# Kernel optimization log

Measured on AMD Instinct MI355X. Metric: run time of the kernel, lower is better.

## Reference

```python
import jax, jax.numpy as jnp
import numpy as np


def setup_inputs() -> dict:
    key = jax.random.key(0)
    k1, k2, k3, k4 = jax.random.split(key, 4)
    bs, n, f_in, f_out, n_head = 4, 2048, 64, 64, 8
    h = jax.random.normal(k1, (bs, n, f_in), dtype=jnp.float32)
    adj = jnp.ones((bs, n, n), dtype=bool)  # accepted by forward but unused
    # xavier-uniform-like init scales
    w = jax.random.uniform(k2, (n_head, f_in, f_out), dtype=jnp.float32,
                           minval=-1.0, maxval=1.0) * np.sqrt(6.0 / (f_in + f_out))
    a_src = jax.random.uniform(k3, (n_head, f_out, 1), dtype=jnp.float32,
                               minval=-1.0, maxval=1.0) * np.sqrt(6.0 / (f_out + 1))
    a_dst = jax.random.uniform(k4, (n_head, f_out, 1), dtype=jnp.float32,
                               minval=-1.0, maxval=1.0) * np.sqrt(6.0 / (f_out + 1))
    bias_p = jnp.zeros((f_out,), dtype=jnp.float32)
    return {"h": h, "adj": adj, "w": w, "a_src": a_src, "a_dst": a_dst, "bias_p": bias_p}


def reference(h, adj, w, a_src, a_dst, bias_p):
    # h: [b, n, f_in], w: [h, f_in, f_out]
    h_prime = jnp.einsum('bnf,hfo->bhno', h, w)          # [b, h, n, f_out]
    t = jnp.tanh(h_prime)
    attn_src = jnp.einsum('bhno,ho->bhn', t, a_src[..., 0])  # [b, h, n]
    attn_dst = jnp.einsum('bhno,ho->bhn', t, a_dst[..., 0])  # [b, h, n]
    # attn[b,h,i,j] = src[b,h,i] + dst[b,h,j]  (dense; adj unused in original)
    attn = attn_src[..., :, None] + attn_dst[..., None, :]   # [b, h, n, n]
    attn = jnp.where(attn >= 0, attn, 0.2 * attn)            # leaky_relu(0.2)
    attn = jax.nn.softmax(attn, axis=-1)
    # dropout p=0.0 -> identity
    out = jnp.einsum('bhij,bhjo->bhio', attn, h_prime)       # [b, h, n, f_out]
    return out + bias_p
```

## Files before the change

### kernel.cpp

```cpp
#include <hip/hip_runtime.h>
#include <hip/hip_bf16.h>

#define NN 2048
#define FF 64
#define NH 8
#define BDIM 4
#define BH 32

typedef __attribute__((ext_vector_type(8))) short short8;
typedef __attribute__((ext_vector_type(4))) float floatx4;
typedef __attribute__((ext_vector_type(4))) unsigned uint4v;

__device__ __forceinline__ float LDIN(const void* p, size_t i, int b16) {
    return b16 ? __bfloat162float(((const __hip_bfloat16*)p)[i]) : ((const float*)p)[i];
}
__device__ __forceinline__ unsigned packhi(float f0, float f1) {
    return __builtin_amdgcn_perm(__float_as_uint(f1), __float_as_uint(f0), 0x07060302);
}
__device__ __forceinline__ float hitrunc(float x) {
    return __uint_as_float(__float_as_uint(x) & 0xFFFF0000u);
}
__device__ __forceinline__ ushort bf16bits(float v) {
    __hip_bfloat16 b = __float2bfloat16(v);
    return __builtin_bit_cast(ushort, b);
}

__global__ __launch_bounds__(256) void k_proj(
    const void* __restrict__ h, const void* __restrict__ w,
    const void* __restrict__ asrc, const void* __restrict__ adst,
    ushort* __restrict__ hpTt, float* __restrict__ esHa, float* __restrict__ esLa,
    float* __restrict__ edHa, float* __restrict__ edLa, int* __restrict__ flagOut)
{
    const int t  = threadIdx.x;
    const int rt = blockIdx.x & 31;
    const int hd = (blockIdx.x >> 5) & 7;
    const int b  = blockIdx.x >> 8;
    const int bh = b * NH + hd;
    const int r0 = rt * 64;

    __shared__ int sb16;
    __shared__ ushort SH[4 * 64 * 72];
    ushort* bHi = SH;
    ushort* bLo = SH + 64 * 72;
    ushort* aHi = SH + 2 * 64 * 72;
    ushort* aLo = SH + 3 * 64 * 72;

    if (t < 64) {
        unsigned word = ((const unsigned*)h)[t];
        unsigned lowexp = (word >> 7) & 0xFFu;
        bool plaus = (lowexp >= 96u && lowexp <= 159u);
        unsigned long long m = __ballot(plaus);
        if (t == 0) sb16 = (__popcll(m) >= 48) ? 1 : 0;
    }
    __syncthreads();
    const int b16 = sb16;
    if (blockIdx.x == 0 && t == 0) flagOut[0] = b16;

    const int lane = t & 63, wv = t >> 6;
    const int ml = lane & 15, q = lane >> 4;

    if (b16) {
        const ushort* wp = (const ushort*)w + (size_t)hd * FF * FF;
        const int n = t & 63, kq4 = (t >> 6) * 4;
#pragma unroll
        for (int g = 0; g < 4; ++g) {
            int kb = g * 16 + kq4;
            ushort v0 = wp[(kb + 0) * FF + n];
            ushort v1 = wp[(kb + 1) * FF + n];
            ushort v2 = wp[(kb + 2) * FF + n];
            ushort v3 = wp[(kb + 3) * FF + n];
            uint2 pk = { (unsigned)v0 | ((unsigned)v1 << 16),
                         (unsigned)v2 | ((unsigned)v3 << 16) };
            *(uint2*)&bHi[n * 72 + kb] = pk;
        }
        const ushort* hsrc = (const ushort*)h + (size_t)(b * NN + r0) * FF;
        for (int g = t; g < 512; g += 256) {
            int row = g >> 3, c8 = (g & 7) * 8;
            uint4v u = *(const uint4v*)(hsrc + row * FF + c8);
            *(uint4v*)&aHi[row * 72 + c8] = u;
        }
    } else {
        const float* wp = (const float*)w + (size_t)hd * FF * FF;
        const int n = t & 63, kq4 = (t >> 6) * 4;
#pragma unroll
        for (int g = 0; g < 4; ++g) {
            int kb = g * 16 + kq4;
            float x0 = wp[(kb + 0) * FF + n];
            float x1 = wp[(kb + 1) * FF + n];
            float x2 = wp[(kb + 2) * FF + n];
            float x3 = wp[(kb + 3) * FF + n];
            uint2 hi2 = { packhi(x0, x1), packhi(x2, x3) };
            uint2 lo2 = { packhi(x0 - hitrunc(x0), x1 - hitrunc(x1)),
                          packhi(x2 - hitrunc(x2), x3 - hitrunc(x3)) };
            *(uint2*)&bHi[n * 72 + kb] = hi2;
            *(uint2*)&bLo[n * 72 + kb] = lo2;
        }
        const float* hsrc = (const float*)h + (size_t)(b * NN + r0) * FF;
        for (int g = t; g < 1024; g += 256) {
            int row = g >> 4, c4 = (g & 15) * 4;
            floatx4 x = *(const floatx4*)(hsrc + row * FF + c4);
            uint2 hi2 = { packhi(x[0], x[1]), packhi(x[2], x[3]) };
            uint2 lo2 = { packhi(x[0] - hitrunc(x[0]), x[1] - hitrunc(x[1])),
                          packhi(x[2] - hitrunc(x[2]), x[3] - hitrunc(x[3])) };
            *(uint2*)&aHi[row * 72 + c4] = hi2;
            *(uint2*)&aLo[row * 72 + c4] = lo2;
        }
    }
    __syncthreads();

    short8 ah[2], al[2];
#pragma unroll
    for (int kc = 0; kc < 2; ++kc) {
        ah[kc] = *(const short8*)&aHi[(wv * 16 + ml) * 72 + kc * 32 + q * 8];
        if (!b16) al[kc] = *(const short8*)&aLo[(wv * 16 + ml) * 72 + kc * 32 + q * 8];
    }
    short8 bhf[4][2], blf[4][2];
#pragma unroll
    for (int nt = 0; nt < 4; ++nt)
#pragma unroll
        for (int kc = 0; kc < 2; ++kc) {
            bhf[nt][kc] = *(const short8*)&bHi[(nt * 16 + ml) * 72 + kc * 32 + q * 8];
            if (!b16) blf[nt][kc] = *(const short8*)&bLo[(nt * 16 + ml) * 72 + kc * 32 + q * 8];
        }

    float aS[4], aD[4];
#pragma unroll
    for (int nt = 0; nt < 4; ++nt) {
        aS[nt] = LDIN(asrc, hd * FF + nt * 16 + ml, b16);
        aD[nt] = LDIN(adst, hd * FF + nt * 16 + ml, b16);
    }

    floatx4 acc[4];
#pragma unroll
    for (int nt = 0; nt < 4; ++nt) {
        floatx4 a = {0.f, 0.f, 0.f, 0.f};
        if (b16) {
#pragma unroll
            for (int kc = 0; kc < 2; ++kc)
                a = __builtin_amdgcn_mfma_f32_16x16x32_bf16(ah[kc], bhf[nt][kc], a, 0, 0, 0);
        } else {
#pragma unroll
            for (int kc = 0; kc < 2; ++kc) {
                a = __builtin_amdgcn_mfma_f32_16x16x32_bf16(ah[kc], bhf[nt][kc], a, 0, 0, 0);
                a = __builtin_amdgcn_mfma_f32_16x16x32_bf16(ah[kc], blf[nt][kc], a, 0, 0, 0);
                a = __builtin_amdgcn_mfma_f32_16x16x32_bf16(al[kc], bhf[nt][kc], a, 0, 0, 0);
            }
        }
        acc[nt] = a;
    }

    __syncthreads();
    ushort* trans = SH;
#pragma unroll
    for (int nt = 0; nt < 4; ++nt) {
        ushort b0 = bf16bits(acc[nt][0]), b1 = bf16bits(acc[nt][1]);
        ushort b2 = bf16bits(acc[nt][2]), b3 = bf16bits(acc[nt][3]);
        uint2 pk = { (unsigned)b0 | ((unsigned)b1 << 16),
                     (unsigned)b2 | ((unsigned)b3 << 16) };
        *(uint2*)&trans[(nt * 16 + ml) * 72 + wv * 16 + q * 4] = pk;
    }

    float ps[4] = {0.f, 0.f, 0.f, 0.f}, pd[4] = {0.f, 0.f, 0.f, 0.f};
#pragma unroll
    for (int nt = 0; nt < 4; ++nt)
#pragma unroll
        for (int reg = 0; reg < 4; ++reg) {
            float tv = tanhf(acc[nt][reg]);
            ps[reg] += tv * aS[nt];
            pd[reg] += tv * aD[nt];
        }
#pragma unroll
    for (int msk = 1; msk < 16; msk <<= 1)
#pragma unroll
        for (int reg = 0; reg < 4; ++reg) {
            ps[reg] += __shfl_xor(ps[reg], msk, 64);
            pd[reg] += __shfl_xor(pd[reg], msk, 64);
        }
    if (ml == 0) {
#pragma unroll
        for (int reg = 0; reg < 4; ++reg) {
            int i = bh * NN + r0 + wv * 16 + q * 4 + reg;
            float sv = ps[reg], dv = pd[reg];
            esHa[i] = __expf(sv);
            esLa[i] = __expf(0.2f * sv);
            edHa[i] = __expf(dv);
            edLa[i] = __expf(0.2f * dv);
        }
    }
    __syncthreads();
    {
        const int o = t >> 2, part = (t & 3) * 16;
        uint4v v0 = *(const uint4v*)&trans[o * 72 + part];
        uint4v v1 = *(const uint4v*)&trans[o * 72 + part + 8];
        ushort* dst = hpTt + (((size_t)bh * 32 + rt) * 64 + o) * 64 + part;
        *(uint4v*)dst = v0;
        *(uint4v*)(dst + 8) = v1;
    }
}

__global__ __launch_bounds__(256) void k_attn(
    const ushort* __restrict__ hpTt,
    const float* __restrict__ esHa, const float* __restrict__ esLa,
    const float* __restrict__ edHa, const float* __restrict__ edLa,
    const void* __restrict__ bias, const int* __restrict__ flag,
    void* __restrict__ out)
{
    const int b16 = flag[0];
    const int t = threadIdx.x;
    const int wv = t >> 6, lane = t & 63;
    const int ml = lane & 15, q = lane >> 4;
    const int bh = blockIdx.x & 31;
    const int ibase = (blockIdx.x >> 5) * 128;
    const int i0 = ibase + wv * 16;

    __shared__ ushort Bc[2][64 * 72];

    const ushort* src = hpTt + (size_t)bh * NN * FF;
    const float* ehp = edHa + bh * NN;
    const float* elp = edLa + bh * NN;

    float es[2], es2[2];
#pragma unroll
    for (int it = 0; it < 2; ++it) {
        es[it]  = esHa[bh * NN + i0 + it * 64 + ml];
        es2[it] = esLa[bh * NN + i0 + it * 64 + ml];
    }

    floatx4 acc[2][4];
#pragma unroll
    for (int it = 0; it < 2; ++it)
#pragma unroll
        for (int nt = 0; nt < 4; ++nt) acc[it][nt] = (floatx4){0.f, 0.f, 0.f, 0.f};
    float den[2] = {0.f, 0.f};

    auto stage = [&](int c, int buf) {
        const ushort* s = src + (size_t)c * 4096 + t * 16;
        uint4v u0 = *(const uint4v*)s;
        uint4v u1 = *(const uint4v*)(s + 8);
        ushort* d = &Bc[buf][(t >> 2) * 72 + (t & 3) * 16];
        *(uint4v*)d = u0;
        *(uint4v*)(d + 8) = u1;
    };

    auto compute = [&](int c, int buf) {
        const int j0 = c * 64;
#pragma unroll
        for (int ks = 0; ks < 2; ++ks) {
            const int col = ks * 32 + q * 8;
            floatx4 eh0 = *(const floatx4*)(ehp + j0 + col);
            floatx4 eh1 = *(const floatx4*)(ehp + j0 + col + 4);
            floatx4 el0 = *(const floatx4*)(elp + j0 + col);
            floatx4 el1 = *(const floatx4*)(elp + j0 + col + 4);
            short8 Bf[4];
#pragma unroll
            for (int nt = 0; nt < 4; ++nt)
                Bf[nt] = *(const short8*)&Bc[buf][(nt * 16 + ml) * 72 + col];
#pragma unroll
            for (int it = 0; it < 2; ++it) {
                float p[8];
#pragma unroll
                for (int j = 0; j < 4; ++j) {
                    p[j]     = fmaxf(es[it] * eh0[j], es2[it] * el0[j]);
                    p[j + 4] = fmaxf(es[it] * eh1[j], es2[it] * el1[j]);
                }
                den[it] += ((p[0] + p[1]) + (p[2] + p[3]))
                         + ((p[4] + p[5]) + (p[6] + p[7]));
                unsigned hw[4], lw[4];
#pragma unroll
                for (int pr = 0; pr < 4; ++pr) {
                    float a0 = p[2 * pr], a1 = p[2 * pr + 1];
                    hw[pr] = packhi(a0, a1);
                    lw[pr] = packhi(a0 - hitrunc(a0), a1 - hitrunc(a1));
                }
                short8 PH = __builtin_bit_cast(short8, (uint4v){hw[0], hw[1], hw[2], hw[3]});
                short8 PL = __builtin_bit_cast(short8, (uint4v){lw[0], lw[1], lw[2], lw[3]});
#pragma unroll
                for (int nt = 0; nt < 4; ++nt) {
                    acc[it][nt] = __builtin_amdgcn_mfma_f32_16x16x32_bf16(PH, Bf[nt], acc[it][nt], 0, 0, 0);
                    acc[it][nt] = __builtin_amdgcn_mfma_f32_16x16x32_bf16(PL, Bf[nt], acc[it][nt], 0, 0, 0);
                }
            }
        }
    };

    stage(0, 0);
    __syncthreads();
    for (int c = 0; c < 32; ++c) {
        const int buf = c & 1;
        if (c < 31) stage(c + 1, buf ^ 1);
        compute(c, buf);
        __syncthreads();
    }

    float biasv[4];
#pragma unroll
    for (int nt = 0; nt < 4; ++nt) biasv[nt] = LDIN(bias, nt * 16 + ml, b16);

#pragma unroll
    for (int it = 0; it < 2; ++it) {
        float d2 = den[it];
        d2 += __shfl_xor(d2, 16, 64);
        d2 += __shfl_xor(d2, 32, 64);
#pragma unroll
        for (int reg = 0; reg < 4; ++reg) {
            float dr = __shfl(d2, q * 4 + reg, 64);
            float inv = 1.0f / dr;
            int i = i0 + it * 64 + q * 4 + reg;
#pragma unroll
            for (int nt = 0; nt < 4; ++nt) {
                float val = acc[it][nt][reg] * inv + biasv[nt];
                size_t oi = ((size_t)bh * NN + i) * FF + nt * 16 + ml;
                if (b16) ((__hip_bfloat16*)out)[oi] = __float2bfloat16(val);
                else     ((float*)out)[oi] = val;
            }
        }
    }
}

extern "C" void kernel_launch(void* const* d_in, const int* in_sizes, int n_in,
                              void* d_out, int out_size, void* d_ws, size_t ws_size,
                              hipStream_t stream) {
    const void* h    = d_in[0];
    const void* w    = d_in[2];
    const void* asrc = d_in[3];
    const void* adst = d_in[4];
    const void* bias = d_in[5];

    float* ws = (float*)d_ws;
    int*    flag = (int*)ws;
    ushort* hpTt = (ushort*)(ws + 16);
    float*  esHa = (float*)(hpTt + (size_t)BH * NN * FF);
    float*  esLa = esHa + BH * NN;
    float*  edHa = esLa + BH * NN;
    float*  edLa = edHa + BH * NN;

    k_proj<<<BDIM * NH * 32, 256, 0, stream>>>(h, w, asrc, adst,
                                               hpTt, esHa, esLa, edHa, edLa, flag);
    k_attn<<<BH * 16, 256, 0, stream>>>(hpTt, esHa, esLa, edHa, edLa,
                                        bias, flag, d_out);
}
```

Measured before the change: 161.5 us.

## Rescale softmax by source factor, drop low-bf16 split, use MFMA for denominator

The attention kernel factors the per-row source exponential out of the softmax, since it cancels in the normalization, leaving one multiply per element against a precomputed exp(-0.8*src) ratio. It drops the hi/lo bf16 split of the probabilities, keeping one MFMA per tile instead of two, and computes the denominator with an extra MFMA against a ones vector. Destination exponentials are staged into shared memory, blocks grow to 512 threads with one row-tile per wave, LDS padding is replaced with an XOR swizzle, and tanh uses an exp/rcp approximation. The changes cut ALU and MFMA work but lower precision of the attention weights to a single bf16 term.

```diff
diff --git a/kernel.cpp b/kernel.cpp
--- a/kernel.cpp
+++ b/kernel.cpp
@@ -24,11 +24,18 @@
     __hip_bfloat16 b = __float2bfloat16(v);
     return __builtin_bit_cast(ushort, b);
 }
+__device__ __forceinline__ int SWZ(int row, int col) {
+    return row * 64 + ((((col >> 3) ^ (row & 7)) << 3) | (col & 7));
+}
+__device__ __forceinline__ float fast_tanh(float v) {
+    float ex = __expf(2.0f * v);
+    return 1.0f - 2.0f * __builtin_amdgcn_rcpf(ex + 1.0f);
+}
 
 __global__ __launch_bounds__(256) void k_proj(
     const void* __restrict__ h, const void* __restrict__ w,
     const void* __restrict__ asrc, const void* __restrict__ adst,
-    ushort* __restrict__ hpTt, float* __restrict__ esHa, float* __restrict__ esLa,
+    ushort* __restrict__ hpTt, float* __restrict__ rArr,
     float* __restrict__ edHa, float* __restrict__ edLa, int* __restrict__ flagOut)
 {
     const int t  = threadIdx.x;
@@ -39,11 +46,11 @@
     const int r0 = rt * 64;
 
     __shared__ int sb16;
-    __shared__ ushort SH[4 * 64 * 72];
+    __shared__ ushort SH[4 * 64 * 64];
     ushort* bHi = SH;
-    ushort* bLo = SH + 64 * 72;
-    ushort* aHi = SH + 2 * 64 * 72;
-    ushort* aLo = SH + 3 * 64 * 72;
+    ushort* bLo = SH + 64 * 64;
+    ushort* aHi = SH + 2 * 64 * 64;
+    ushort* aLo = SH + 3 * 64 * 64;
 
     if (t < 64) {
         unsigned word = ((const unsigned*)h)[t];
@@ -71,13 +78,13 @@
             ushort v3 = wp[(kb + 3) * FF + n];
             uint2 pk = { (unsigned)v0 | ((unsigned)v1 << 16),
                          (unsigned)v2 | ((unsigned)v3 << 16) };
-            *(uint2*)&bHi[n * 72 + kb] = pk;
+            *(uint2*)&bHi[SWZ(n, kb)] = pk;
         }
         const ushort* hsrc = (const ushort*)h + (size_t)(b * NN + r0) * FF;
         for (int g = t; g < 512; g += 256) {
             int row = g >> 3, c8 = (g & 7) * 8;
             uint4v u = *(const uint4v*)(hsrc + row * FF + c8);
-            *(uint4v*)&aHi[row * 72 + c8] = u;
+            *(uint4v*)&aHi[SWZ(row, c8)] = u;
         }
     } else {
         const float* wp = (const float*)w + (size_t)hd * FF * FF;
@@ -92,8 +99,8 @@
             uint2 hi2 = { packhi(x0, x1), packhi(x2, x3) };
             uint2 lo2 = { packhi(x0 - hitrunc(x0), x1 - hitrunc(x1)),
                           packhi(x2 - hitrunc(x2), x3 - hitrunc(x3)) };
-            *(uint2*)&bHi[n * 72 + kb] = hi2;
-            *(uint2*)&bLo[n * 72 + kb] = lo2;
+            *(uint2*)&bHi[SWZ(n, kb)] = hi2;
+            *(uint2*)&bLo[SWZ(n, kb)] = lo2;
         }
         const float* hsrc = (const float*)h + (size_t)(b * NN + r0) * FF;
         for (int g = t; g < 1024; g += 256) {
@@ -102,8 +109,8 @@
             uint2 hi2 = { packhi(x[0], x[1]), packhi(x[2], x[3]) };
             uint2 lo2 = { packhi(x[0] - hitrunc(x[0]), x[1] - hitrunc(x[1])),
                           packhi(x[2] - hitrunc(x[2]), x[3] - hitrunc(x[3])) };
-            *(uint2*)&aHi[row * 72 + c4] = hi2;
-            *(uint2*)&aLo[row * 72 + c4] = lo2;
+            *(uint2*)&aHi[SWZ(row, c4)] = hi2;
+            *(uint2*)&aLo[SWZ(row, c4)] = lo2;
         }
     }
     __syncthreads();
@@ -111,16 +118,16 @@
     short8 ah[2], al[2];
 #pragma unroll
     for (int kc = 0; kc < 2; ++kc) {
-        ah[kc] = *(const short8*)&aHi[(wv * 16 + ml) * 72 + kc * 32 + q * 8];
-        if (!b16) al[kc] = *(const short8*)&aLo[(wv * 16 + ml) * 72 + kc * 32 + q * 8];
+        ah[kc] = *(const short8*)&aHi[SWZ(wv * 16 + ml, kc * 32 + q * 8)];
+        if (!b16) al[kc] = *(const short8*)&aLo[SWZ(wv * 16 + ml, kc * 32 + q * 8)];
     }
     short8 bhf[4][2], blf[4][2];
 #pragma unroll
     for (int nt = 0; nt < 4; ++nt)
 #pragma unroll
         for (int kc = 0; kc < 2; ++kc) {
-            bhf[nt][kc] = *(const short8*)&bHi[(nt * 16 + ml) * 72 + kc * 32 + q * 8];
-            if (!b16) blf[nt][kc] = *(const short8*)&bLo[(nt * 16 + ml) * 72 + kc * 32 + q * 8];
+            bhf[nt][kc] = *(const short8*)&bHi[SWZ(nt * 16 + ml, kc * 32 + q * 8)];
+            if (!b16) blf[nt][kc] = *(const short8*)&bLo[SWZ(nt * 16 + ml, kc * 32 + q * 8)];
         }
 
     float aS[4], aD[4];
@@ -157,7 +164,7 @@
         ushort b2 = bf16bits(acc[nt][2]), b3 = bf16bits(acc[nt][3]);
         uint2 pk = { (unsigned)b0 | ((unsigned)b1 << 16),
                      (unsigned)b2 | ((unsigned)b3 << 16) };
-        *(uint2*)&trans[(nt * 16 + ml) * 72 + wv * 16 + q * 4] = pk;
+        *(uint2*)&trans[SWZ(nt * 16 + ml, wv * 16 + q * 4)] = pk;
     }
 
     float ps[4] = {0.f, 0.f, 0.f, 0.f}, pd[4] = {0.f, 0.f, 0.f, 0.f};
@@ -165,7 +172,7 @@
     for (int nt = 0; nt < 4; ++nt)
 #pragma unroll
         for (int reg = 0; reg < 4; ++reg) {
-            float tv = tanhf(acc[nt][reg]);
+            float tv = fast_tanh(acc[nt][reg]);
             ps[reg] += tv * aS[nt];
             pd[reg] += tv * aD[nt];
         }
@@ -181,8 +188,7 @@
         for (int reg = 0; reg < 4; ++reg) {
             int i = bh * NN + r0 + wv * 16 + q * 4 + reg;
             float sv = ps[reg], dv = pd[reg];
-            esHa[i] = __expf(sv);
-            esLa[i] = __expf(0.2f * sv);
+            rArr[i] = __expf(-0.8f * sv);
             edHa[i] = __expf(dv);
             edLa[i] = __expf(0.2f * dv);
         }
@@ -190,17 +196,16 @@
     __syncthreads();
     {
         const int o = t >> 2, part = (t & 3) * 16;
-        uint4v v0 = *(const uint4v*)&trans[o * 72 + part];
-        uint4v v1 = *(const uint4v*)&trans[o * 72 + part + 8];
+        uint4v v0 = *(const uint4v*)&trans[SWZ(o, part)];
+        uint4v v1 = *(const uint4v*)&trans[SWZ(o, part + 8)];
         ushort* dst = hpTt + (((size_t)bh * 32 + rt) * 64 + o) * 64 + part;
         *(uint4v*)dst = v0;
         *(uint4v*)(dst + 8) = v1;
     }
 }
 
-__global__ __launch_bounds__(256) void k_attn(
-    const ushort* __restrict__ hpTt,
-    const float* __restrict__ esHa, const float* __restrict__ esLa,
+__global__ __launch_bounds__(512) void k_attn(
+    const ushort* __restrict__ hpTt, const float* __restrict__ rArr,
     const float* __restrict__ edHa, const float* __restrict__ edLa,
     const void* __restrict__ bias, const int* __restrict__ flag,
     void* __restrict__ out)
@@ -210,36 +215,29 @@
     const int wv = t >> 6, lane = t & 63;
     const int ml = lane & 15, q = lane >> 4;
     const int bh = blockIdx.x & 31;
-    const int ibase = (blockIdx.x >> 5) * 128;
-    const int i0 = ibase + wv * 16;
-
-    __shared__ ushort Bc[2][64 * 72];
+    const int i0 = (blockIdx.x >> 5) * 128 + wv * 16;
+
+    __shared__ ushort Bc[2][64 * 64];
+    __shared__ __align__(16) float ehS[NN];
+    __shared__ __align__(16) float elS[NN];
+
+    ((floatx4*)ehS)[t] = ((const floatx4*)(edHa + bh * NN))[t];
+    ((floatx4*)elS)[t] = ((const floatx4*)(edLa + bh * NN))[t];
 
     const ushort* src = hpTt + (size_t)bh * NN * FF;
-    const float* ehp = edHa + bh * NN;
-    const float* elp = edLa + bh * NN;
-
-    float es[2], es2[2];
-#pragma unroll
-    for (int it = 0; it < 2; ++it) {
-        es[it]  = esHa[bh * NN + i0 + it * 64 + ml];
-        es2[it] = esLa[bh * NN + i0 + it * 64 + ml];
-    }
-
-    floatx4 acc[2][4];
-#pragma unroll
-    for (int it = 0; it < 2; ++it)
-#pragma unroll
-        for (int nt = 0; nt < 4; ++nt) acc[it][nt] = (floatx4){0.f, 0.f, 0.f, 0.f};
-    float den[2] = {0.f, 0.f};
+    const float r = rArr[bh * NN + i0 + ml];
+
+    const short8 ONESB = {0x3F80, 0x3F80, 0x3F80, 0x3F80,
+                          0x3F80, 0x3F80, 0x3F80, 0x3F80};
+
+    floatx4 acc[4];
+#pragma unroll
+    for (int nt = 0; nt < 4; ++nt) acc[nt] = (floatx4){0.f, 0.f, 0.f, 0.f};
+    floatx4 accD = {0.f, 0.f, 0.f, 0.f};
 
     auto stage = [&](int c, int buf) {
-        const ushort* s = src + (size_t)c * 4096 + t * 16;
-        uint4v u0 = *(const uint4v*)s;
-        uint4v u1 = *(const uint4v*)(s + 8);
-        ushort* d = &Bc[buf][(t >> 2) * 72 + (t & 3) * 16];
-        *(uint4v*)d = u0;
-        *(uint4v*)(d + 8) = u1;
+        uint4v u = *(const uint4v*)(src + (size_t)c * 4096 + t * 8);
+        *(uint4v*)&Bc[buf][SWZ(t >> 3, (t & 7) * 8)] = u;
     };
 
     auto compute = [&](int c, int buf) {
@@ -247,39 +245,27 @@
 #pragma unroll
         for (int ks = 0; ks < 2; ++ks) {
             const int col = ks * 32 + q * 8;
-            floatx4 eh0 = *(const floatx4*)(ehp + j0 + col);
-            floatx4 eh1 = *(const floatx4*)(ehp + j0 + col + 4);
-            floatx4 el0 = *(const floatx4*)(elp + j0 + col);
-            floatx4 el1 = *(const floatx4*)(elp + j0 + col + 4);
+            floatx4 eh0 = *(const floatx4*)&ehS[j0 + col];
+            floatx4 eh1 = *(const floatx4*)&ehS[j0 + col + 4];
+            floatx4 el0 = *(const floatx4*)&elS[j0 + col];
+            floatx4 el1 = *(const floatx4*)&elS[j0 + col + 4];
             short8 Bf[4];
 #pragma unroll
             for (int nt = 0; nt < 4; ++nt)
-                Bf[nt] = *(const short8*)&Bc[buf][(nt * 16 + ml) * 72 + col];
-#pragma unroll
-            for (int it = 0; it < 2; ++it) {
-                float p[8];
-#pragma unroll
-                for (int j = 0; j < 4; ++j) {
-                    p[j]     = fmaxf(es[it] * eh0[j], es2[it] * el0[j]);
-                    p[j + 4] = fmaxf(es[it] * eh1[j], es2[it] * el1[j]);
-                }
-                den[it] += ((p[0] + p[1]) + (p[2] + p[3]))
-                         + ((p[4] + p[5]) + (p[6] + p[7]));
-                unsigned hw[4], lw[4];
-#pragma unroll
-                for (int pr = 0; pr < 4; ++pr) {
-                    float a0 = p[2 * pr], a1 = p[2 * pr + 1];
-                    hw[pr] = packhi(a0, a1);
-                    lw[pr] = packhi(a0 - hitrunc(a0), a1 - hitrunc(a1));
-                }
-                short8 PH = __builtin_bit_cast(short8, (uint4v){hw[0], hw[1], hw[2], hw[3]});
-                short8 PL = __builtin_bit_cast(short8, (uint4v){lw[0], lw[1], lw[2], lw[3]});
-#pragma unroll
-                for (int nt = 0; nt < 4; ++nt) {
-                    acc[it][nt] = __builtin_amdgcn_mfma_f32_16x16x32_bf16(PH, Bf[nt], acc[it][nt], 0, 0, 0);
-                    acc[it][nt] = __builtin_amdgcn_mfma_f32_16x16x32_bf16(PL, Bf[nt], acc[it][nt], 0, 0, 0);
-                }
+                Bf[nt] = *(const short8*)&Bc[buf][SWZ(nt * 16 + ml, col)];
+            float p[8];
+#pragma unroll
+            for (int j = 0; j < 4; ++j) {
+                p[j]     = fmaxf(eh0[j], r * el0[j]);
+                p[j + 4] = fmaxf(eh1[j], r * el1[j]);
             }
+            uint4v hv = { packhi(p[0], p[1]), packhi(p[2], p[3]),
+                          packhi(p[4], p[5]), packhi(p[6], p[7]) };
+            short8 PH = __builtin_bit_cast(short8, hv);
+#pragma unroll
+            for (int nt = 0; nt < 4; ++nt)
+                acc[nt] = __builtin_amdgcn_mfma_f32_16x16x32_bf16(PH, Bf[nt], acc[nt], 0, 0, 0);
+            accD = __builtin_amdgcn_mfma_f32_16x16x32_bf16(PH, ONESB, accD, 0, 0, 0);
         }
     };
 
@@ -297,22 +283,15 @@
     for (int nt = 0; nt < 4; ++nt) biasv[nt] = LDIN(bias, nt * 16 + ml, b16);
 
 #pragma unroll
-    for (int it = 0; it < 2; ++it) {
-        float d2 = den[it];
-        d2 += __shfl_xor(d2, 16, 64);
-        d2 += __shfl_xor(d2, 32, 64);
-#pragma unroll
-        for (int reg = 0; reg < 4; ++reg) {
-            float dr = __shfl(d2, q * 4 + reg, 64);
-            float inv = 1.0f / dr;
-            int i = i0 + it * 64 + q * 4 + reg;
-#pragma unroll
-            for (int nt = 0; nt < 4; ++nt) {
-                float val = acc[it][nt][reg] * inv + biasv[nt];
-                size_t oi = ((size_t)bh * NN + i) * FF + nt * 16 + ml;
-                if (b16) ((__hip_bfloat16*)out)[oi] = __float2bfloat16(val);
-                else     ((float*)out)[oi] = val;
-            }
+    for (int reg = 0; reg < 4; ++reg) {
+        float inv = 1.0f / accD[reg];
+        int i = i0 + q * 4 + reg;
+#pragma unroll
+        for (int nt = 0; nt < 4; ++nt) {
+            float val = acc[nt][reg] * inv + biasv[nt];
+            size_t oi = ((size_t)bh * NN + i) * FF + nt * 16 + ml;
+            if (b16) ((__hip_bfloat16*)out)[oi] = __float2bfloat16(val);
+            else     ((float*)out)[oi] = val;
         }
     }
 }
@@ -329,13 +308,12 @@
     float* ws = (float*)d_ws;
     int*    flag = (int*)ws;
     ushort* hpTt = (ushort*)(ws + 16);
-    float*  esHa = (float*)(hpTt + (size_t)BH * NN * FF);
-    float*  esLa = esHa + BH * NN;
-    float*  edHa = esLa + BH * NN;
+    float*  rArr = (float*)(hpTt + (size_t)BH * NN * FF);
+    float*  edHa = rArr + BH * NN;
     float*  edLa = edHa + BH * NN;
 
     k_proj<<<BDIM * NH * 32, 256, 0, stream>>>(h, w, asrc, adst,
-                                               hpTt, esHa, esLa, edHa, edLa, flag);
-    k_attn<<<BH * 16, 256, 0, stream>>>(hpTt, esHa, esLa, edHa, edLa,
+                                               hpTt, rArr, edHa, edLa, flag);
+    k_attn<<<BH * 16, 512, 0, stream>>>(hpTt, rArr, edHa, edLa,
                                         bias, flag, d_out);
 }
```

Result: faster. 139.8 us (-13.5%).
